# Optimization experiments

Hardware: AMD Instinct MI355X
Metric: run time of the kernel (lower is better)

## Reference

```python
import jax, jax.numpy as jnp
import numpy as np

RAD2DEG = 180.0 / 3.14159  # module uses 3.14159, not pi

def _conv2d(x, w):
    # x: (N,1,H,W), w: (O,1,3,3), SAME padding, stride 1
    return jax.lax.conv_general_dilated(
        x, w, window_strides=(1, 1), padding='SAME',
        dimension_numbers=('NCHW', 'OIHW', 'NCHW'))

def _make_filters():
    sobel = np.array([[1, 0, -1], [2, 0, -2], [1, 0, -1]], dtype=np.float32)
    f0   = [[0,0,0],[0,1,-1],[0,0,0]]
    f45  = [[0,0,0],[0,1,0],[0,0,-1]]
    f90  = [[0,0,0],[0,1,0],[0,-1,0]]
    f135 = [[0,0,0],[0,1,0],[-1,0,0]]
    f180 = [[0,0,0],[-1,1,0],[0,0,0]]
    f225 = [[-1,0,0],[0,1,0],[0,0,0]]
    f270 = [[0,-1,0],[0,1,0],[0,0,0]]
    f315 = [[0,0,-1],[0,1,0],[0,0,0]]
    dirs = np.stack([f0,f45,f90,f135,f180,f225,f270,f315]).astype(np.float32)
    return sobel, dirs

def setup_inputs() -> dict:
    key = jax.random.key(0)
    H, W = 2160, 3840
    img = jax.random.uniform(key, (1, 3, H, W), dtype=jnp.float32)
    sobel, dirs = _make_filters()
    sobel_h = jnp.asarray(sobel)[None, None]          # (1,1,3,3)
    sobel_v = jnp.asarray(sobel.T)[None, None]        # (1,1,3,3)
    dir_w = jnp.asarray(dirs)[:, None]                # (8,1,3,3)
    return {"img": img, "sobel_h": sobel_h, "sobel_v": sobel_v, "dir_w": dir_w}

def reference(img, sobel_h, sobel_v, dir_w):
    # grayscale: mean of the 3 channels
    gray = (img[:, 0:1] + img[:, 1:2] + img[:, 2:3]) / 3.0        # (1,1,H,W)
    grad_x = _conv2d(gray, sobel_h)
    grad_y = _conv2d(gray, sobel_v)
    grad_mag = jnp.sqrt(grad_x ** 2 + grad_y ** 2)                # (1,1,H,W)
    # orientation in degrees, snapped to multiples of 45 (round-half-even, like torch.round)
    ori = jnp.round((jnp.arctan2(grad_y, grad_x) * RAD2DEG + 180.0) / 45.0)
    idx_pos = jnp.mod(ori, 8.0).astype(jnp.int32)                 # (1,1,H,W)
    idx_neg = jnp.mod(ori + 4.0, 8.0).astype(jnp.int32)
    all_filtered = _conv2d(grad_mag, dir_w)                       # (1,8,H,W)
    # per-pixel channel select (the flattened gather in the original)
    pos = jnp.take_along_axis(all_filtered, idx_pos, axis=1)      # (1,1,H,W)
    neg = jnp.take_along_axis(all_filtered, idx_neg, axis=1)
    is_max = jnp.minimum(pos, neg) > 0.0
    # in-place aliasing in the original: thin_edges/early_threshold alias grad_mag,
    # so the final binary map is: is_max AND (grad_mag >= 0.2)
    th = jnp.where(is_max & (grad_mag >= 0.2), 1.0, 0.0).astype(jnp.float32)
    return th
```

## Files before the change

### kernel.cpp

```cpp
#include <hip/hip_runtime.h>
#include <math.h>

#define IMG_W 3840
#define IMG_H 2160
#define OUTW  60
#define R     20
#define ITERS (R + 4)
#define MROWS (R + 2)

#define DXPACK 0x901A
#define DYPACK 0x1A9

#define T1_SLOPE 0.41421317376456f
#define T2_SLOPE 2.41420676743300f
#define SECT_EPS 3.0e-5f

__device__ __noinline__ int slow_sector(float sx, float sy) {
#pragma clang fp contract(off)
    const float RADF = (float)(180.0 / 3.14159);
    float t = atan2f(sy, sx);
    float wv = ((t * RADF) + 180.0f) / 45.0f;
    float ori = rintf(wv);
    float fr = fabsf(wv - ori);
    if (fr > 0.4995f) {
        double td = atan2((double)sy, (double)sx);
        float t2 = (float)td;
        wv = ((t2 * RADF) + 180.0f) / 45.0f;
        ori = rintf(wv);
    }
    return ((int)ori) & 7;
}

__global__ __launch_bounds__(256, 4) void canny_like_kernel(const float* __restrict__ img,
                                                            float* __restrict__ out) {
#pragma clang fp contract(off)
    __shared__ float lds_m[4][MROWS][64];

    const int lane = threadIdx.x;
    const int w    = threadIdx.y;
    const int X0   = (blockIdx.x * 4 + w) * OUTW;
    const int Y0   = blockIdx.y * R;
    const int x    = X0 - 2 + lane;
    const bool xok    = (unsigned)x < (unsigned)IMG_W;
    const int  xc     = min(max(x, 0), IMG_W - 1);
    const bool xmok   = (lane >= 1) && (lane <= 62) && xok;
    const bool xoutok = (lane >= 2) && (lane <= 61);

    const float* im1 = img + (size_t)IMG_W * IMG_H;
    const float* im2 = img + 2 * (size_t)IMG_W * IMG_H;

    float gl[3], gc[3], gr[3];
    float mc_p = 0.0f;
    int   off_p = 0;

#pragma unroll
    for (int k = 0; k < ITERS; ++k) {
        const int y = Y0 - 2 + k;
        float g = 0.0f;
        if ((unsigned)y < (unsigned)IMG_H) {
            int o = y * IMG_W + xc;
            float c0 = img[o], c1 = im1[o], c2 = im2[o];
            float t = ((c0 + c1) + c2) / 3.0f;
            g = xok ? t : 0.0f;
        }
        const int s = k % 3;
        gc[s] = g;
        gl[s] = __shfl_up(g, 1);
        gr[s] = __shfl_down(g, 1);

        if (k >= 2) {
            const int i0 = (k - 2) % 3, i1 = (k - 1) % 3, i2 = k % 3;
            float a00 = gl[i0], a01 = gc[i0], a02 = gr[i0];
            float a10 = gl[i1],               a12 = gr[i1];
            float a20 = gl[i2], a21 = gc[i2], a22 = gr[i2];
            float sx = a00;
            sx = sx - a02;
            sx = sx + 2.0f * a10;
            sx = sx - 2.0f * a12;
            sx = sx + a20;
            sx = sx - a22;
            float sy = a00;
            sy = sy + 2.0f * a01;
            sy = sy + a02;
            sy = sy - a20;
            sy = sy - 2.0f * a21;
            sy = sy - a22;
            float magv = sqrtf(sx * sx + sy * sy);

            float ax = fabsf(sx), ay = fabsf(sy);
            float d1 = fmaf(-T1_SLOPE, ax, ay);
            float d2 = fmaf(-T2_SLOPE, ax, ay);
            float sA = ax + ay;
            int dxo, dyo;
            if (__builtin_expect(fabsf(d1) < SECT_EPS * sA || fabsf(d2) < SECT_EPS * sA, 0)) {
                int idx = slow_sector(sx, sy);
                dxo = ((DXPACK >> (2 * idx)) & 3) - 1;
                dyo = ((DYPACK >> (2 * idx)) & 3) - 1;
            } else {
                dxo = (d2 > 0.0f) ? 0 : ((sx > 0.0f) ? -1 : 1);
                dyo = (d1 < 0.0f) ? 0 : ((sy > 0.0f) ? -1 : 1);
            }
            const bool vok = xmok && ((unsigned)(y - 1) < (unsigned)IMG_H);
            float mag = vok ? magv : 0.0f;
            int  offv = vok ? (dyo * 64 + dxo) : 0;

            lds_m[w][k - 2][lane] = mag;

            if (k >= 4) {
                const float* cb = &lds_m[w][k - 3][lane];
                float mp = cb[off_p];
                float mn = cb[-off_p];
                float res = (fminf(mc_p - mp, mc_p - mn) > 0.0f && mc_p >= 0.2f) ? 1.0f : 0.0f;
                if (xoutok)
                    out[(size_t)(Y0 + k - 4) * IMG_W + x] = res;
            }
            mc_p = mag;
            off_p = offv;
        }
    }
}

extern "C" void kernel_launch(void* const* d_in, const int* in_sizes, int n_in,
                              void* d_out, int out_size, void* d_ws, size_t ws_size,
                              hipStream_t stream) {
    const float* img = (const float*)d_in[0];
    float* out = (float*)d_out;
    dim3 grid(64 / 4, IMG_H / R);
    dim3 block(64, 4);
    canny_like_kernel<<<grid, block, 0, stream>>>(img, out);
}
```

Baseline: 166.4 us.

## Preload all grayscale rows up front and use a 4-row LDS ring buffer

Hoists all 24 rows of three-channel loads into a register array before the compute loop, using clamped row indices so the loads are unconditional and can all be in flight together. The per-wave magnitude buffer in LDS shrinks from 22 rows to a 4-row ring buffer addressed with wraparound masking, which cuts shared-memory use per block. This raises register pressure from holding 24 gray values, which may hurt occupancy under the existing launch bounds.

```diff
diff --git a/kernel.cpp b/kernel.cpp
--- a/kernel.cpp
+++ b/kernel.cpp
@@ -5,7 +5,7 @@
 #define IMG_H 2160
 #define OUTW  60
 #define R     20
-#define ITERS (R + 4)
+#define GROWS (R + 4)
 #define MROWS (R + 2)
 
 #define DXPACK 0x901A
@@ -34,7 +34,7 @@
 __global__ __launch_bounds__(256, 4) void canny_like_kernel(const float* __restrict__ img,
                                                             float* __restrict__ out) {
 #pragma clang fp contract(off)
-    __shared__ float lds_m[4][MROWS][64];
+    __shared__ float lds_m[4][4][64];
 
     const int lane = threadIdx.x;
     const int w    = threadIdx.y;
@@ -49,74 +49,81 @@
     const float* im1 = img + (size_t)IMG_W * IMG_H;
     const float* im2 = img + 2 * (size_t)IMG_W * IMG_H;
 
-    float gl[3], gc[3], gr[3];
-    float mc_p = 0.0f;
+    float g[GROWS];
+#pragma unroll
+    for (int k = 0; k < GROWS; ++k) {
+        const int  y   = Y0 - 2 + k;
+        const bool yok = (unsigned)y < (unsigned)IMG_H;
+        const int  yc  = min(max(y, 0), IMG_H - 1);
+        const int  o   = yc * IMG_W + xc;
+        float c0 = img[o], c1 = im1[o], c2 = im2[o];
+        float t = ((c0 + c1) + c2) / 3.0f;
+        g[k] = (xok && yok) ? t : 0.0f;
+    }
+
+    float* const B = &lds_m[w][0][0];
+
+    float gl[3], gr[3];
+    gl[0] = __shfl_up(g[0], 1);  gr[0] = __shfl_down(g[0], 1);
+    gl[1] = __shfl_up(g[1], 1);  gr[1] = __shfl_down(g[1], 1);
+
+    float mc_p  = 0.0f;
     int   off_p = 0;
 
 #pragma unroll
-    for (int k = 0; k < ITERS; ++k) {
-        const int y = Y0 - 2 + k;
-        float g = 0.0f;
-        if ((unsigned)y < (unsigned)IMG_H) {
-            int o = y * IMG_W + xc;
-            float c0 = img[o], c1 = im1[o], c2 = im2[o];
-            float t = ((c0 + c1) + c2) / 3.0f;
-            g = xok ? t : 0.0f;
+    for (int m = 0; m < MROWS; ++m) {
+        const int i0 = m % 3, i1 = (m + 1) % 3, i2 = (m + 2) % 3;
+        gl[i2] = __shfl_up(g[m + 2], 1);
+        gr[i2] = __shfl_down(g[m + 2], 1);
+
+        float a00 = gl[i0], a01 = g[m],     a02 = gr[i0];
+        float a10 = gl[i1],                 a12 = gr[i1];
+        float a20 = gl[i2], a21 = g[m + 2], a22 = gr[i2];
+        float sx = a00;
+        sx = sx - a02;
+        sx = sx + 2.0f * a10;
+        sx = sx - 2.0f * a12;
+        sx = sx + a20;
+        sx = sx - a22;
+        float sy = a00;
+        sy = sy + 2.0f * a01;
+        sy = sy + a02;
+        sy = sy - a20;
+        sy = sy - 2.0f * a21;
+        sy = sy - a22;
+        float magv = sqrtf(sx * sx + sy * sy);
+
+        float ax = fabsf(sx), ay = fabsf(sy);
+        float d1 = fmaf(-T1_SLOPE, ax, ay);
+        float d2 = fmaf(-T2_SLOPE, ax, ay);
+        float sA = ax + ay;
+        int dxo, dyo;
+        if (__builtin_expect(fabsf(d1) < SECT_EPS * sA || fabsf(d2) < SECT_EPS * sA, 0)) {
+            int idx = slow_sector(sx, sy);
+            dxo = ((DXPACK >> (2 * idx)) & 3) - 1;
+            dyo = ((DYPACK >> (2 * idx)) & 3) - 1;
+        } else {
+            dxo = (d2 > 0.0f) ? 0 : ((sx > 0.0f) ? -1 : 1);
+            dyo = (d1 < 0.0f) ? 0 : ((sy > 0.0f) ? -1 : 1);
         }
-        const int s = k % 3;
-        gc[s] = g;
-        gl[s] = __shfl_up(g, 1);
-        gr[s] = __shfl_down(g, 1);
+        const bool vok = xmok && ((unsigned)(Y0 - 1 + m) < (unsigned)IMG_H);
+        float mag  = vok ? magv : 0.0f;
+        int   offv = vok ? (dyo * 64 + dxo) : 0;
 
-        if (k >= 2) {
-            const int i0 = (k - 2) % 3, i1 = (k - 1) % 3, i2 = k % 3;
-            float a00 = gl[i0], a01 = gc[i0], a02 = gr[i0];
-            float a10 = gl[i1],               a12 = gr[i1];
-            float a20 = gl[i2], a21 = gc[i2], a22 = gr[i2];
-            float sx = a00;
-            sx = sx - a02;
-            sx = sx + 2.0f * a10;
-            sx = sx - 2.0f * a12;
-            sx = sx + a20;
-            sx = sx - a22;
-            float sy = a00;
-            sy = sy + 2.0f * a01;
-            sy = sy + a02;
-            sy = sy - a20;
-            sy = sy - 2.0f * a21;
-            sy = sy - a22;
-            float magv = sqrtf(sx * sx + sy * sy);
+        B[(m & 3) * 64 + lane] = mag;
 
-            float ax = fabsf(sx), ay = fabsf(sy);
-            float d1 = fmaf(-T1_SLOPE, ax, ay);
-            float d2 = fmaf(-T2_SLOPE, ax, ay);
-            float sA = ax + ay;
-            int dxo, dyo;
-            if (__builtin_expect(fabsf(d1) < SECT_EPS * sA || fabsf(d2) < SECT_EPS * sA, 0)) {
-                int idx = slow_sector(sx, sy);
-                dxo = ((DXPACK >> (2 * idx)) & 3) - 1;
-                dyo = ((DYPACK >> (2 * idx)) & 3) - 1;
-            } else {
-                dxo = (d2 > 0.0f) ? 0 : ((sx > 0.0f) ? -1 : 1);
-                dyo = (d1 < 0.0f) ? 0 : ((sy > 0.0f) ? -1 : 1);
-            }
-            const bool vok = xmok && ((unsigned)(y - 1) < (unsigned)IMG_H);
-            float mag = vok ? magv : 0.0f;
-            int  offv = vok ? (dyo * 64 + dxo) : 0;
-
-            lds_m[w][k - 2][lane] = mag;
-
-            if (k >= 4) {
-                const float* cb = &lds_m[w][k - 3][lane];
-                float mp = cb[off_p];
-                float mn = cb[-off_p];
-                float res = (fminf(mc_p - mp, mc_p - mn) > 0.0f && mc_p >= 0.2f) ? 1.0f : 0.0f;
-                if (xoutok)
-                    out[(size_t)(Y0 + k - 4) * IMG_W + x] = res;
-            }
-            mc_p = mag;
-            off_p = offv;
+        if (m >= 2) {
+            const int rp  = ((m - 1) & 3) * 64;
+            const int ipp = (rp + lane + off_p) & 255;
+            const int ipn = (rp + lane - off_p) & 255;
+            float mp = B[ipp];
+            float mn = B[ipn];
+            float res = (fminf(mc_p - mp, mc_p - mn) > 0.0f && mc_p >= 0.2f) ? 1.0f : 0.0f;
+            if (xoutok)
+                out[(size_t)(Y0 + m - 2) * IMG_W + x] = res;
         }
+        mc_p  = mag;
+        off_p = offv;
     }
 }
 
```

Result: no change. 164.6 us (-1.1%).
